# Kernel optimization log

Hardware: AMD Instinct MI355X
Metric: run time of the kernel (lower is better)

The kernel has to match this reference:

```python
import jax, jax.numpy as jnp
import numpy as np

N = 100000      # nodes
E = 1000000     # edges
IN = 64         # in_dim
TD = 64         # time_dim
OUT = 64        # out_dim
H = 4           # num_heads
HD = OUT // H   # head_dim = 16


def setup_inputs() -> dict:
    key = jax.random.key(0)
    ks = jax.random.split(key, 12)
    g = lambda k, shp, s: (jax.random.normal(k, shp, jnp.float32) * s)
    return {
        "x": g(ks[0], (N, IN), 1.0),
        "time_features": g(ks[1], (N, TD), 1.0),
        "edge_index": jax.random.randint(ks[2], (2, E), 0, N, dtype=jnp.int32),
        # nn.Linear weights stored as [in, out] (already transposed)
        "q_w": g(ks[3], (IN + TD, OUT), 0.05), "q_b": g(ks[4], (OUT,), 0.05),
        "k_w": g(ks[5], (IN + TD, OUT), 0.05), "k_b": g(ks[6], (OUT,), 0.05),
        "v_w": g(ks[7], (IN, OUT), 0.05),      "v_b": g(ks[8], (OUT,), 0.05),
        "o_w": g(ks[9], (OUT, OUT), 0.05),     "o_b": g(ks[10], (OUT,), 0.05),
    }


def reference(x, time_features, edge_index, q_w, q_b, k_w, k_b, v_w, v_b, o_w, o_b):
    xt = jnp.concatenate([x, time_features], axis=-1)            # [N, IN+TD]
    Q = (xt @ q_w + q_b).reshape(N, H, HD)
    K = (xt @ k_w + k_b).reshape(N, H, HD)
    V = (x @ v_w + v_b).reshape(N, H, HD)
    src, dst = edge_index[0], edge_index[1]
    # edge-gather QK dot-product: [E, H]
    scores = jnp.sum(Q[dst] * K[src], axis=-1) / np.float32(np.sqrt(HD))
    # per-destination (segment) softmax over edges, numerically stable two-pass
    seg_max = jax.ops.segment_max(scores, dst, num_segments=N)   # [N, H]
    e = jnp.exp(scores - seg_max[dst])                           # [E, H]
    seg_sum = jax.ops.segment_sum(e, dst, num_segments=N)        # [N, H]
    attn = e / seg_sum[dst]                                      # [E, H]
    # weighted scatter-add of values
    messages = attn[..., None] * V[src]                          # [E, H, HD]
    out = jax.ops.segment_sum(messages, dst, num_segments=N)     # [N, H, HD]
    out = out.reshape(N, OUT)
    return out @ o_w + o_b
```

## Files before the change

kernel.cpp:

```cpp
#include <hip/hip_runtime.h>
#include <hip/hip_fp16.h>
#include <math.h>

#define N_NODES 100000
#define N_EDGES 1000000
#define QKV_BLOCKS ((N_NODES + 63) / 64)
#define FILL_BLOCKS ((N_EDGES + 255) / 256)
#define PREP_BLOCKS 96
#define AGG_BLOCKS ((N_NODES + 63) / 64)

typedef __attribute__((ext_vector_type(8))) _Float16 f16x8;
typedef __attribute__((ext_vector_type(4))) float    f32x4;

__global__ __launch_bounds__(256) void prep_kernel(
    const float* __restrict__ qw, const float* __restrict__ kw,
    const float* __restrict__ vw, const float* __restrict__ ow,
    _Float16* __restrict__ WqT, _Float16* __restrict__ WkT,
    _Float16* __restrict__ WvT, _Float16* __restrict__ WoT)
{
    const int idx = blockIdx.x * 256 + threadIdx.x;
    if (idx < 8192) {
        const int c = idx >> 7, k = idx & 127;
        WqT[idx] = (_Float16)qw[k * 64 + c];
    } else if (idx < 16384) {
        const int i = idx - 8192, c = i >> 7, k = i & 127;
        WkT[i] = (_Float16)kw[k * 64 + c];
    } else if (idx < 20480) {
        const int i = idx - 16384, c = i >> 6, k = i & 63;
        WvT[i] = (_Float16)vw[k * 64 + c];
    } else {
        const int i = idx - 20480, c = i >> 6, k = i & 63;
        WoT[i] = (_Float16)ow[k * 64 + c];
    }
}

__global__ __launch_bounds__(256) void fill_qkv_kernel(
    const int* __restrict__ src, const int* __restrict__ dst,
    int* __restrict__ head, int2* __restrict__ next2,
    const float* __restrict__ x, const float* __restrict__ tf,
    const _Float16* __restrict__ WqT, const _Float16* __restrict__ WkT,
    const _Float16* __restrict__ WvT,
    const float* __restrict__ qb, const float* __restrict__ kb,
    const float* __restrict__ vb,
    _Float16* __restrict__ Qh, _Float16* __restrict__ KV)
{
    __shared__ _Float16 xt[64][128];
    const int t = threadIdx.x;

    if (blockIdx.x >= QKV_BLOCKS) {
        const int e = (blockIdx.x - QKV_BLOCKS) * 256 + t;
        if (e < N_EDGES) {
            const int d  = dst[e];
            const int sv = src[e];
            const int old = atomicExch(&head[d], e);
            next2[e] = make_int2(old, sv);
        }
        return;
    }

    const int base = blockIdx.x * 64;

    {
        const int j = t & 15;
        #pragma unroll
        for (int i = 0; i < 4; ++i) {
            const int r = (t >> 4) + 16 * i;
            int node = base + r;
            if (node >= N_NODES) node = N_NODES - 1;
            const float* p = (j < 8) ? (x  + (size_t)node * 64 + 8 * j)
                                     : (tf + (size_t)node * 64 + 8 * (j - 8));
            const float4 lo = ((const float4*)p)[0];
            const float4 hi = ((const float4*)p)[1];
            f16x8 h = { (_Float16)lo.x, (_Float16)lo.y, (_Float16)lo.z,
                        (_Float16)lo.w, (_Float16)hi.x, (_Float16)hi.y,
                        (_Float16)hi.z, (_Float16)hi.w };
            const int js = j ^ (r & 15);
            *(f16x8*)&xt[r][js * 8] = h;
        }
    }

    const int wave = t >> 6;
    const int lane = t & 63;
    const int lrow = lane & 15;
    const int lgrp = lane >> 4;
    const int cw   = wave * 16;

    f16x8 bq[4], bk[4], bv[2];
    const float biasq = qb[cw + lrow];
    const float biask = kb[cw + lrow];
    const float biasv = vb[cw + lrow];
    {
        const size_t rq = (size_t)(cw + lrow) * 128 + lgrp * 8;
        #pragma unroll
        for (int kt = 0; kt < 4; ++kt) {
            bq[kt] = *(const f16x8*)&WqT[rq + kt * 32];
            bk[kt] = *(const f16x8*)&WkT[rq + kt * 32];
        }
        const size_t rv = (size_t)(cw + lrow) * 64 + lgrp * 8;
        #pragma unroll
        for (int kt = 0; kt < 2; ++kt)
            bv[kt] = *(const f16x8*)&WvT[rv + kt * 32];
    }
    __syncthreads();

    #pragma unroll
    for (int rt = 0; rt < 4; ++rt) {
        f16x8 a[4];
        const int r = rt * 16 + lrow;
        #pragma unroll
        for (int kt = 0; kt < 4; ++kt) {
            const int js = (kt * 4 + lgrp) ^ lrow;
            a[kt] = *(const f16x8*)&xt[r][js * 8];
        }
        f32x4 accq = {0.f, 0.f, 0.f, 0.f};
        f32x4 acck = {0.f, 0.f, 0.f, 0.f};
        f32x4 accv = {0.f, 0.f, 0.f, 0.f};
        #pragma unroll
        for (int kt = 0; kt < 4; ++kt) {
            accq = __builtin_amdgcn_mfma_f32_16x16x32_f16(a[kt], bq[kt], accq, 0, 0, 0);
            acck = __builtin_amdgcn_mfma_f32_16x16x32_f16(a[kt], bk[kt], acck, 0, 0, 0);
        }
        #pragma unroll
        for (int kt = 0; kt < 2; ++kt)
            accv = __builtin_amdgcn_mfma_f32_16x16x32_f16(a[kt], bv[kt], accv, 0, 0, 0);
        #pragma unroll
        for (int rr = 0; rr < 4; ++rr) {
            const int node = base + rt * 16 + lgrp * 4 + rr;
            if (node < N_NODES) {
                Qh[(size_t)node * 64 + cw + lrow]        = (_Float16)(accq[rr] + biasq);
                KV[(size_t)node * 128 + cw + lrow]       = (_Float16)(acck[rr] + biask);
                KV[(size_t)node * 128 + 64 + cw + lrow]  = (_Float16)(accv[rr] + biasv);
            }
        }
    }
}

__global__ __launch_bounds__(256) void agg_kernel(
    const int* __restrict__ head, const int2* __restrict__ next2,
    const __half* __restrict__ Qh, const __half* __restrict__ KVh,
    const _Float16* __restrict__ WoT, const float* __restrict__ ob,
    float* __restrict__ out)
{
    __shared__ _Float16 aggh[64][64];
    __shared__ int pool[4];
    const int t    = threadIdx.x;
    const int wave = t >> 6;
    const int lane = t & 63;
    const int g    = lane >> 3;
    const int s    = lane & 7;
    const int lrow = lane & 15;
    const int lgrp = lane >> 4;
    const int cw   = wave * 16;
    const int nb   = blockIdx.x * 64;
    const int wbase = wave * 16;

    if (lane == 0) pool[wave] = 8;

    f16x8 bo0, bo1;
    {
        const size_t ro = (size_t)(cw + lrow) * 64 + lgrp * 8;
        bo0 = *(const f16x8*)&WoT[ro];
        bo1 = *(const f16x8*)&WoT[ro + 32];
    }
    const float biaso = ob[cw + lrow];
    __syncthreads();

    const uint4* __restrict__ Q4  = (const uint4*)Qh;
    const uint4* __restrict__ KV4 = (const uint4*)KVh;

    int   idx  = g;
    int   cur  = nb + wbase + idx;
    int   e    = (cur < N_NODES) ? head[cur] : -1;
    bool  done = false;
    float acc[8] = {0.f, 0.f, 0.f, 0.f, 0.f, 0.f, 0.f, 0.f};
    float ssum = 0.f;
    float qf[8];
    {
        const int qn = (cur < N_NODES) ? cur : 0;
        const uint4 qu = Q4[(size_t)qn * 8 + s];
        const __half2* qh = (const __half2*)&qu;
        #pragma unroll
        for (int j = 0; j < 4; ++j) {
            const float2 a = __half22float2(qh[j]);
            qf[2 * j] = a.x; qf[2 * j + 1] = a.y;
        }
    }

    for (;;) {
        while (e < 0 && !done) {
            const float inv = (ssum > 0.f) ? (1.0f / ssum) : 0.0f;
            const int r = wbase + idx;
            f16x8 h = { (_Float16)(acc[0] * inv), (_Float16)(acc[1] * inv),
                        (_Float16)(acc[2] * inv), (_Float16)(acc[3] * inv),
                        (_Float16)(acc[4] * inv), (_Float16)(acc[5] * inv),
                        (_Float16)(acc[6] * inv), (_Float16)(acc[7] * inv) };
            *(f16x8*)&aggh[r][(s ^ (r & 7)) * 8] = h;

            int tkt = 0;
            if (s == 0) tkt = atomicAdd(&pool[wave], 1);
            tkt = __shfl(tkt, g * 8);
            if (tkt < 16) {
                idx = tkt;
                cur = nb + wbase + idx;
                e   = (cur < N_NODES) ? head[cur] : -1;
                const int qn = (cur < N_NODES) ? cur : 0;
                const uint4 qu = Q4[(size_t)qn * 8 + s];
                const __half2* qh = (const __half2*)&qu;
                #pragma unroll
                for (int j = 0; j < 4; ++j) {
                    const float2 a = __half22float2(qh[j]);
                    qf[2 * j] = a.x; qf[2 * j + 1] = a.y;
                }
                #pragma unroll
                for (int j = 0; j < 8; ++j) acc[j] = 0.f;
                ssum = 0.f;
            } else {
                done = true;
            }
        }
        if (__all(done)) break;

        const bool act = (e >= 0);
        const int  es  = act ? e : 0;
        const int2 sn  = next2[es];
        const int  sv  = sn.y;
        const uint4 ku = KV4[(size_t)sv * 16 + s];
        const uint4 vu = KV4[(size_t)sv * 16 + 8 + s];

        float kf[8], vf[8];
        {
            const __half2* kh = (const __half2*)&ku;
            const __half2* vh = (const __half2*)&vu;
            #pragma unroll
            for (int j = 0; j < 4; ++j) {
                const float2 a = __half22float2(kh[j]);
                const float2 b = __half22float2(vh[j]);
                kf[2 * j] = a.x; kf[2 * j + 1] = a.y;
                vf[2 * j] = b.x; vf[2 * j + 1] = b.y;
            }
        }
        float dq = qf[0] * kf[0] + qf[1] * kf[1] + qf[2] * kf[2] + qf[3] * kf[3]
                 + qf[4] * kf[4] + qf[5] * kf[5] + qf[6] * kf[6] + qf[7] * kf[7];
        dq += __shfl_xor(dq, 1);
        const float p = act ? __expf(dq * 0.25f) : 0.f;
        ssum += p;
        #pragma unroll
        for (int j = 0; j < 8; ++j) acc[j] = fmaf(p, vf[j], acc[j]);
        e = act ? sn.x : e;
    }
    __syncthreads();

    #pragma unroll
    for (int rt = 0; rt < 4; ++rt) {
        const int r = rt * 16 + lrow;
        f16x8 a0 = *(const f16x8*)&aggh[r][((lgrp)     ^ (lrow & 7)) * 8];
        f16x8 a1 = *(const f16x8*)&aggh[r][((4 + lgrp) ^ (lrow & 7)) * 8];
        f32x4 acco = {0.f, 0.f, 0.f, 0.f};
        acco = __builtin_amdgcn_mfma_f32_16x16x32_f16(a0, bo0, acco, 0, 0, 0);
        acco = __builtin_amdgcn_mfma_f32_16x16x32_f16(a1, bo1, acco, 0, 0, 0);
        #pragma unroll
        for (int rr = 0; rr < 4; ++rr) {
            const int n = nb + rt * 16 + lgrp * 4 + rr;
            if (n < N_NODES)
                out[(size_t)n * 64 + cw + lrow] = acco[rr] + biaso;
        }
    }
}

extern "C" void kernel_launch(void* const* d_in, const int* in_sizes, int n_in,
                              void* d_out, int out_size, void* d_ws, size_t ws_size,
                              hipStream_t stream) {
    const float* x  = (const float*)d_in[0];
    const float* tf = (const float*)d_in[1];
    const int*   ei = (const int*)  d_in[2];
    const float* qw = (const float*)d_in[3];
    const float* qb = (const float*)d_in[4];
    const float* kw = (const float*)d_in[5];
    const float* kb = (const float*)d_in[6];
    const float* vw = (const float*)d_in[7];
    const float* vb = (const float*)d_in[8];
    const float* ow = (const float*)d_in[9];
    const float* ob = (const float*)d_in[10];
    float* out = (float*)d_out;

    char* ws = (char*)d_ws;
    const size_t hf = (size_t)N_NODES * 64 * sizeof(_Float16);

    _Float16* Qh      = (_Float16*)(ws);
    _Float16* KV      = (_Float16*)(ws + hf);
    _Float16* WqT     = (_Float16*)(ws + 3 * hf);
    _Float16* WkT     = WqT + 8192;
    _Float16* WvT     = WkT + 8192;
    _Float16* WoT     = WvT + 4096;
    int*      head    = (int*)(WoT + 4096);
    int2*     next2   = (int2*)(head + N_NODES);

    const int* src = ei;
    const int* dst = ei + N_EDGES;

    const dim3 blk(256);

    hipMemsetAsync(head, 0xFF, N_NODES * sizeof(int), stream);

    prep_kernel<<<dim3(PREP_BLOCKS), blk, 0, stream>>>(
        qw, kw, vw, ow, WqT, WkT, WvT, WoT);

    fill_qkv_kernel<<<dim3(QKV_BLOCKS + FILL_BLOCKS), blk, 0, stream>>>(
        src, dst, head, next2,
        x, tf, WqT, WkT, WvT, qb, kb, vb, Qh, KV);

    agg_kernel<<<dim3(AGG_BLOCKS), blk, 0, stream>>>(
        head, next2, (const __half*)Qh, (const __half*)KV, WoT, ob, out);
}
```

Before: 131.8 us.

## Split linked-list fill by destination range to overlap with aggregation

Splits destination nodes at a fixed boundary. Edges pointing to nodes in the first range are linked during the QKV kernel. Edges pointing to the remaining nodes are linked inside a new combined kernel, which aggregates the first range at the same time, and a third kernel then aggregates the remaining nodes. The aim is to overlap part of the edge-list construction with aggregation work so GPU slack is better used. In exchange the dst array is read twice, which adds a kernel launch and a redundant full pass over the edges.

```diff
diff --git a/kernel.cpp b/kernel.cpp
--- a/kernel.cpp
+++ b/kernel.cpp
@@ -4,10 +4,12 @@
 
 #define N_NODES 100000
 #define N_EDGES 1000000
+#define DSPLIT 70016
 #define QKV_BLOCKS ((N_NODES + 63) / 64)
 #define FILL_BLOCKS ((N_EDGES + 255) / 256)
 #define PREP_BLOCKS 96
-#define AGG_BLOCKS ((N_NODES + 63) / 64)
+#define AGG_A_BLOCKS (DSPLIT / 64)
+#define AGG_B_BLOCKS ((N_NODES - DSPLIT + 63) / 64)
 
 typedef __attribute__((ext_vector_type(8))) _Float16 f16x8;
 typedef __attribute__((ext_vector_type(4))) float    f32x4;
@@ -34,115 +36,27 @@
     }
 }
 
-__global__ __launch_bounds__(256) void fill_qkv_kernel(
+__device__ __forceinline__ void fill_role(
+    const int e, const int dlo, const int dhi,
     const int* __restrict__ src, const int* __restrict__ dst,
-    int* __restrict__ head, int2* __restrict__ next2,
-    const float* __restrict__ x, const float* __restrict__ tf,
-    const _Float16* __restrict__ WqT, const _Float16* __restrict__ WkT,
-    const _Float16* __restrict__ WvT,
-    const float* __restrict__ qb, const float* __restrict__ kb,
-    const float* __restrict__ vb,
-    _Float16* __restrict__ Qh, _Float16* __restrict__ KV)
-{
-    __shared__ _Float16 xt[64][128];
-    const int t = threadIdx.x;
-
-    if (blockIdx.x >= QKV_BLOCKS) {
-        const int e = (blockIdx.x - QKV_BLOCKS) * 256 + t;
-        if (e < N_EDGES) {
-            const int d  = dst[e];
-            const int sv = src[e];
+    int* __restrict__ head, int2* __restrict__ next2)
+{
+    if (e < N_EDGES) {
+        const int d = dst[e];
+        if (d >= dlo && d < dhi) {
             const int old = atomicExch(&head[d], e);
-            next2[e] = make_int2(old, sv);
-        }
-        return;
-    }
-
-    const int base = blockIdx.x * 64;
-
-    {
-        const int j = t & 15;
-        #pragma unroll
-        for (int i = 0; i < 4; ++i) {
-            const int r = (t >> 4) + 16 * i;
-            int node = base + r;
-            if (node >= N_NODES) node = N_NODES - 1;
-            const float* p = (j < 8) ? (x  + (size_t)node * 64 + 8 * j)
-                                     : (tf + (size_t)node * 64 + 8 * (j - 8));
-            const float4 lo = ((const float4*)p)[0];
-            const float4 hi = ((const float4*)p)[1];
-            f16x8 h = { (_Float16)lo.x, (_Float16)lo.y, (_Float16)lo.z,
-                        (_Float16)lo.w, (_Float16)hi.x, (_Float16)hi.y,
-                        (_Float16)hi.z, (_Float16)hi.w };
-            const int js = j ^ (r & 15);
-            *(f16x8*)&xt[r][js * 8] = h;
-        }
-    }
-
-    const int wave = t >> 6;
-    const int lane = t & 63;
-    const int lrow = lane & 15;
-    const int lgrp = lane >> 4;
-    const int cw   = wave * 16;
-
-    f16x8 bq[4], bk[4], bv[2];
-    const float biasq = qb[cw + lrow];
-    const float biask = kb[cw + lrow];
-    const float biasv = vb[cw + lrow];
-    {
-        const size_t rq = (size_t)(cw + lrow) * 128 + lgrp * 8;
-        #pragma unroll
-        for (int kt = 0; kt < 4; ++kt) {
-            bq[kt] = *(const f16x8*)&WqT[rq + kt * 32];
-            bk[kt] = *(const f16x8*)&WkT[rq + kt * 32];
-        }
-        const size_t rv = (size_t)(cw + lrow) * 64 + lgrp * 8;
-        #pragma unroll
-        for (int kt = 0; kt < 2; ++kt)
-            bv[kt] = *(const f16x8*)&WvT[rv + kt * 32];
-    }
-    __syncthreads();
-
-    #pragma unroll
-    for (int rt = 0; rt < 4; ++rt) {
-        f16x8 a[4];
-        const int r = rt * 16 + lrow;
-        #pragma unroll
-        for (int kt = 0; kt < 4; ++kt) {
-            const int js = (kt * 4 + lgrp) ^ lrow;
-            a[kt] = *(const f16x8*)&xt[r][js * 8];
-        }
-        f32x4 accq = {0.f, 0.f, 0.f, 0.f};
-        f32x4 acck = {0.f, 0.f, 0.f, 0.f};
-        f32x4 accv = {0.f, 0.f, 0.f, 0.f};
-        #pragma unroll
-        for (int kt = 0; kt < 4; ++kt) {
-            accq = __builtin_amdgcn_mfma_f32_16x16x32_f16(a[kt], bq[kt], accq, 0, 0, 0);
-            acck = __builtin_amdgcn_mfma_f32_16x16x32_f16(a[kt], bk[kt], acck, 0, 0, 0);
-        }
-        #pragma unroll
-        for (int kt = 0; kt < 2; ++kt)
-            accv = __builtin_amdgcn_mfma_f32_16x16x32_f16(a[kt], bv[kt], accv, 0, 0, 0);
-        #pragma unroll
-        for (int rr = 0; rr < 4; ++rr) {
-            const int node = base + rt * 16 + lgrp * 4 + rr;
-            if (node < N_NODES) {
-                Qh[(size_t)node * 64 + cw + lrow]        = (_Float16)(accq[rr] + biasq);
-                KV[(size_t)node * 128 + cw + lrow]       = (_Float16)(acck[rr] + biask);
-                KV[(size_t)node * 128 + 64 + cw + lrow]  = (_Float16)(accv[rr] + biasv);
-            }
-        }
-    }
-}
-
-__global__ __launch_bounds__(256) void agg_kernel(
+            next2[e] = make_int2(old, src[e]);
+        }
+    }
+}
+
+__device__ __forceinline__ void agg_role(
+    const int nb, _Float16 (*aggh)[64], int* pool,
     const int* __restrict__ head, const int2* __restrict__ next2,
     const __half* __restrict__ Qh, const __half* __restrict__ KVh,
     const _Float16* __restrict__ WoT, const float* __restrict__ ob,
     float* __restrict__ out)
 {
-    __shared__ _Float16 aggh[64][64];
-    __shared__ int pool[4];
     const int t    = threadIdx.x;
     const int wave = t >> 6;
     const int lane = t & 63;
@@ -151,7 +65,6 @@
     const int lrow = lane & 15;
     const int lgrp = lane >> 4;
     const int cw   = wave * 16;
-    const int nb   = blockIdx.x * 64;
     const int wbase = wave * 16;
 
     if (lane == 0) pool[wave] = 8;
@@ -267,6 +180,133 @@
     }
 }
 
+__global__ __launch_bounds__(256) void fill_qkv_kernel(
+    const int* __restrict__ src, const int* __restrict__ dst,
+    int* __restrict__ head, int2* __restrict__ next2,
+    const float* __restrict__ x, const float* __restrict__ tf,
+    const _Float16* __restrict__ WqT, const _Float16* __restrict__ WkT,
+    const _Float16* __restrict__ WvT,
+    const float* __restrict__ qb, const float* __restrict__ kb,
+    const float* __restrict__ vb,
+    _Float16* __restrict__ Qh, _Float16* __restrict__ KV)
+{
+    __shared__ _Float16 xt[64][128];
+    const int t = threadIdx.x;
+
+    if (blockIdx.x >= QKV_BLOCKS) {
+        fill_role((blockIdx.x - QKV_BLOCKS) * 256 + t, 0, DSPLIT,
+                  src, dst, head, next2);
+        return;
+    }
+
+    const int base = blockIdx.x * 64;
+
+    {
+        const int j = t & 15;
+        #pragma unroll
+        for (int i = 0; i < 4; ++i) {
+            const int r = (t >> 4) + 16 * i;
+            int node = base + r;
+            if (node >= N_NODES) node = N_NODES - 1;
+            const float* p = (j < 8) ? (x  + (size_t)node * 64 + 8 * j)
+                                     : (tf + (size_t)node * 64 + 8 * (j - 8));
+            const float4 lo = ((const float4*)p)[0];
+            const float4 hi = ((const float4*)p)[1];
+            f16x8 h = { (_Float16)lo.x, (_Float16)lo.y, (_Float16)lo.z,
+                        (_Float16)lo.w, (_Float16)hi.x, (_Float16)hi.y,
+                        (_Float16)hi.z, (_Float16)hi.w };
+            const int js = j ^ (r & 15);
+            *(f16x8*)&xt[r][js * 8] = h;
+        }
+    }
+
+    const int wave = t >> 6;
+    const int lane = t & 63;
+    const int lrow = lane & 15;
+    const int lgrp = lane >> 4;
+    const int cw   = wave * 16;
+
+    f16x8 bq[4], bk[4], bv[2];
+    const float biasq = qb[cw + lrow];
+    const float biask = kb[cw + lrow];
+    const float biasv = vb[cw + lrow];
+    {
+        const size_t rq = (size_t)(cw + lrow) * 128 + lgrp * 8;
+        #pragma unroll
+        for (int kt = 0; kt < 4; ++kt) {
+            bq[kt] = *(const f16x8*)&WqT[rq + kt * 32];
+            bk[kt] = *(const f16x8*)&WkT[rq + kt * 32];
+        }
+        const size_t rv = (size_t)(cw + lrow) * 64 + lgrp * 8;
+        #pragma unroll
+        for (int kt = 0; kt < 2; ++kt)
+            bv[kt] = *(const f16x8*)&WvT[rv + kt * 32];
+    }
+    __syncthreads();
+
+    #pragma unroll
+    for (int rt = 0; rt < 4; ++rt) {
+        f16x8 a[4];
+        const int r = rt * 16 + lrow;
+        #pragma unroll
+        for (int kt = 0; kt < 4; ++kt) {
+            const int js = (kt * 4 + lgrp) ^ lrow;
+            a[kt] = *(const f16x8*)&xt[r][js * 8];
+        }
+        f32x4 accq = {0.f, 0.f, 0.f, 0.f};
+        f32x4 acck = {0.f, 0.f, 0.f, 0.f};
+        f32x4 accv = {0.f, 0.f, 0.f, 0.f};
+        #pragma unroll
+        for (int kt = 0; kt < 4; ++kt) {
+            accq = __builtin_amdgcn_mfma_f32_16x16x32_f16(a[kt], bq[kt], accq, 0, 0, 0);
+            acck = __builtin_amdgcn_mfma_f32_16x16x32_f16(a[kt], bk[kt], acck, 0, 0, 0);
+        }
+        #pragma unroll
+        for (int kt = 0; kt < 2; ++kt)
+            accv = __builtin_amdgcn_mfma_f32_16x16x32_f16(a[kt], bv[kt], accv, 0, 0, 0);
+        #pragma unroll
+        for (int rr = 0; rr < 4; ++rr) {
+            const int node = base + rt * 16 + lgrp * 4 + rr;
+            if (node < N_NODES) {
+                Qh[(size_t)node * 64 + cw + lrow]        = (_Float16)(accq[rr] + biasq);
+                KV[(size_t)node * 128 + cw + lrow]       = (_Float16)(acck[rr] + biask);
+                KV[(size_t)node * 128 + 64 + cw + lrow]  = (_Float16)(accv[rr] + biasv);
+            }
+        }
+    }
+}
+
+__global__ __launch_bounds__(256) void agg_fill_kernel(
+    const int* __restrict__ src, const int* __restrict__ dst,
+    int* __restrict__ head, int2* __restrict__ next2,
+    const __half* __restrict__ Qh, const __half* __restrict__ KVh,
+    const _Float16* __restrict__ WoT, const float* __restrict__ ob,
+    float* __restrict__ out)
+{
+    __shared__ _Float16 aggh[64][64];
+    __shared__ int pool[4];
+
+    if (blockIdx.x >= AGG_A_BLOCKS) {
+        fill_role((blockIdx.x - AGG_A_BLOCKS) * 256 + threadIdx.x,
+                  DSPLIT, N_NODES, src, dst, head, next2);
+        return;
+    }
+    agg_role(blockIdx.x * 64, aggh, pool,
+             head, next2, Qh, KVh, WoT, ob, out);
+}
+
+__global__ __launch_bounds__(256) void agg_kernel(
+    const int* __restrict__ head, const int2* __restrict__ next2,
+    const __half* __restrict__ Qh, const __half* __restrict__ KVh,
+    const _Float16* __restrict__ WoT, const float* __restrict__ ob,
+    float* __restrict__ out)
+{
+    __shared__ _Float16 aggh[64][64];
+    __shared__ int pool[4];
+    agg_role(DSPLIT + blockIdx.x * 64, aggh, pool,
+             head, next2, Qh, KVh, WoT, ob, out);
+}
+
 extern "C" void kernel_launch(void* const* d_in, const int* in_sizes, int n_in,
                               void* d_out, int out_size, void* d_ws, size_t ws_size,
                               hipStream_t stream) {
@@ -309,6 +349,10 @@
         src, dst, head, next2,
         x, tf, WqT, WkT, WvT, qb, kb, vb, Qh, KV);
 
-    agg_kernel<<<dim3(AGG_BLOCKS), blk, 0, stream>>>(
+    agg_fill_kernel<<<dim3(AGG_A_BLOCKS + FILL_BLOCKS), blk, 0, stream>>>(
+        src, dst, head, next2,
+        (const __half*)Qh, (const __half*)KV, WoT, ob, out);
+
+    agg_kernel<<<dim3(AGG_B_BLOCKS), blk, 0, stream>>>(
         head, next2, (const __half*)Qh, (const __half*)KV, WoT, ob, out);
 }
```

Measured after the change: 149.6 us. +13.5%, slower.
